# Optimization experiments

Measured on AMD Instinct MI355X. Metric: run time of the kernel, lower is better.

The kernel has to match this reference:

```python
import jax, jax.numpy as jnp
import numpy as np
from jax import lax


def _conv(x, w, b, pad, dil):
    # standard dense conv, NCHW / OIHW
    out = lax.conv_general_dilated(
        x, w, window_strides=(1, 1), padding=[(pad, pad), (pad, pad)],
        rhs_dilation=(dil, dil), dimension_numbers=('NCHW', 'OIHW', 'NCHW'))
    return out + b[None, :, None, None]


def _bilinear_sample(x, py, px):
    # x: [B,C,H,W]; py,px: [B,H,W] float coords. Zero padding outside bounds
    # (matches torchvision deform_conv2d bilinear sampling).
    B, C, H, W = x.shape
    y0 = jnp.floor(py)
    x0 = jnp.floor(px)
    wy = (py - y0)[:, None]  # [B,1,H,W]
    wx = (px - x0)[:, None]
    y0i = y0.astype(jnp.int32)
    x0i = x0.astype(jnp.int32)
    xf = x.reshape(B, C, H * W)

    def gather(yi, xi):
        valid = ((yi >= 0) & (yi < H) & (xi >= 0) & (xi < W))[:, None]
        yc = jnp.clip(yi, 0, H - 1)
        xc = jnp.clip(xi, 0, W - 1)
        idx = jnp.broadcast_to((yc * W + xc).reshape(B, 1, H * W), (B, C, H * W))
        v = jnp.take_along_axis(xf, idx, axis=2).reshape(B, C, H, W)
        return v * valid.astype(x.dtype)

    v00 = gather(y0i, x0i)
    v01 = gather(y0i, x0i + 1)
    v10 = gather(y0i + 1, x0i)
    v11 = gather(y0i + 1, x0i + 1)
    return (v00 * (1 - wy) * (1 - wx) + v01 * (1 - wy) * wx
            + v10 * wy * (1 - wx) + v11 * wy * wx)


def _deform_dw_conv(x, off_w, off_b, dw_w, k, pad, dil):
    # offset net: regular conv -> [B, 2*k*k, H, W] (dy,dx per kernel tap)
    # then depthwise deformable conv with weight dw_w: [C,1,k,k], no bias.
    B, C, H, W = x.shape
    off = _conv(x, off_w, off_b, pad, dil).reshape(B, k * k, 2, H, W)
    ys = jnp.arange(H, dtype=x.dtype)[None, :, None]  # [1,H,1]
    xs = jnp.arange(W, dtype=x.dtype)[None, None, :]  # [1,1,W]
    out = jnp.zeros_like(x)
    for t in range(k * k):  # small fixed tap count (25 or 49)
        ki, kj = t // k, t % k
        py = ys - pad + ki * dil + off[:, t, 0]  # [B,H,W]
        px = xs - pad + kj * dil + off[:, t, 1]
        samp = _bilinear_sample(x, py, px)       # [B,C,H,W]
        out = out + samp * dw_w[:, 0, ki, kj][None, :, None, None]
    return out


def setup_inputs() -> dict:
    key = jax.random.key(0)
    ks = jax.random.split(key, 10)
    B, C, H, W = 8, 64, 128, 128
    x = jax.random.normal(ks[0], (B, C, H, W), dtype=jnp.float32)
    # conv0: DeformConv 5x5, pad=2, dil=1, depthwise
    off0_w = jax.random.normal(ks[1], (2 * 25, C, 5, 5), dtype=jnp.float32) * 0.01
    off0_b = jnp.zeros((2 * 25,), dtype=jnp.float32)
    dw0_w = jax.random.normal(ks[2], (C, 1, 5, 5), dtype=jnp.float32) * (1.0 / 5.0)
    # conv_spatial: DeformConv 7x7, pad=9, dil=3, depthwise
    off1_w = jax.random.normal(ks[3], (2 * 49, C, 7, 7), dtype=jnp.float32) * 0.01
    off1_b = jnp.zeros((2 * 49,), dtype=jnp.float32)
    dw1_w = jax.random.normal(ks[4], (C, 1, 7, 7), dtype=jnp.float32) * (1.0 / 7.0)
    # conv1: 1x1 dense conv with bias
    conv1_w = jax.random.normal(ks[5], (C, C, 1, 1), dtype=jnp.float32) * (1.0 / np.sqrt(C))
    conv1_b = jnp.zeros((C,), dtype=jnp.float32)
    return {"x": x, "off0_w": off0_w, "off0_b": off0_b, "dw0_w": dw0_w,
            "off1_w": off1_w, "off1_b": off1_b, "dw1_w": dw1_w,
            "conv1_w": conv1_w, "conv1_b": conv1_b}


def reference(x, off0_w, off0_b, dw0_w, off1_w, off1_b, dw1_w, conv1_w, conv1_b):
    u = x
    attn = _deform_dw_conv(x, off0_w, off0_b, dw0_w, k=5, pad=2, dil=1)
    attn = _deform_dw_conv(attn, off1_w, off1_b, dw1_w, k=7, pad=9, dil=3)
    attn = jnp.einsum('bchw,oc->bohw', attn, conv1_w[:, :, 0, 0]) + conv1_b[None, :, None, None]
    return u * attn
```

## Files before the change

kernel.cpp:

```cpp
#include <hip/hip_runtime.h>

#define Bb 8
#define C  64
#define Hh 128
#define Ww 128
#define HW (Hh * Ww)

typedef __attribute__((ext_vector_type(8))) short b16x8;
typedef __attribute__((ext_vector_type(4))) float f32x4;
typedef _Float16 f16x8 __attribute__((ext_vector_type(8)));
typedef _Float16 h2 __attribute__((ext_vector_type(2)));
typedef __fp16 fp16x2cv __attribute__((ext_vector_type(2)));

__device__ __forceinline__ ushort f2h(float f) {
    union { _Float16 h; ushort u; } z; z.h = (_Float16)f; return z.u;
}
__device__ __forceinline__ h2 u2h(uint u) {
    union { uint u; h2 h; } x; x.u = u; return x.h;
}
__device__ __forceinline__ uint h2u(h2 h) {
    union { uint u; h2 h; } x; x.h = h; return x.u;
}
__device__ __forceinline__ uint pkrtz_u(float a, float b) {
    union { fp16x2cv h; uint u; } z;
    z.h = __builtin_amdgcn_cvt_pkrtz(a, b); return z.u;
}
__device__ __forceinline__ f16x8 s2h8(b16x8 s) {
    union { b16x8 s; f16x8 h; } x; x.s = s; return x.h;
}

__global__ void pack_nhwc(const float* __restrict__ in, ushort* __restrict__ out) {
    __shared__ ushort t[64][65];
    const int bx = blockIdx.x;
    const int b = bx >> 8, rem = bx & 255, h = rem >> 1, w0 = (rem & 1) << 6;
    const int x = threadIdx.x, wl = x & 63, cs = x >> 6;
    const float* ip = in + (((size_t)b * 64) << 14) + (h << 7) + w0 + wl;
    #pragma unroll
    for (int i = 0; i < 16; ++i) {
        const int c = i * 4 + cs;
        t[wl][c] = f2h(ip[(size_t)c << 14]);
    }
    __syncthreads();
    ushort* op = out + ((size_t)((b * Hh + h) * Ww + w0)) * 64 + wl;
    #pragma unroll
    for (int i = 0; i < 16; ++i) {
        const int w = i * 4 + cs;
        op[(size_t)w * 64] = t[w][wl];
    }
}

__global__ void pack_w(const float* __restrict__ src, ushort* __restrict__ dst,
                       int OC, int OCP, int KK, int n) {
    const int idx = blockIdx.x * 256 + threadIdx.x;
    if (idx >= n) return;
    const int kk = idx & 31;
    const int oc = (idx >> 5) % OCP;
    const int s = idx / (32 * OCP);
    const int c = (s & 1) * 32 + kk;
    const int t = s >> 1;
    const float v = (oc < OC) ? src[((size_t)oc * 64 + c) * KK + t] : 0.f;
    dst[idx] = f2h(v);
}

__global__ void pack_dwt(const float* __restrict__ src, ushort* __restrict__ dst, int KK) {
    const int i = blockIdx.x * 256 + threadIdx.x;
    if (i < KK * 64) {
        const int t = i >> 6, ch = i & 63;
        dst[i] = f2h(src[ch * KK + t]);
    }
}

template<int K, int PAD, int DIL, int OCP, int KR>
__global__ __launch_bounds__(256, 2) void conv_mfma(
    const ushort* __restrict__ xp,
    const ushort* __restrict__ wp,
    const float* __restrict__ bias,
    ushort* __restrict__ outp) {
    constexpr int WIDTH = 64 + (K - 1) * DIL;
    constexpr int S = 2 * K * K;
    constexpr int NT = OCP / 16;
    constexpr int TPW = (NT + 3) / 4;
    __shared__ __align__(16) ushort lds[KR * WIDTH * 64];

    const int bx = blockIdx.x;
    const int b = bx >> 8, rem = bx & 255, h = rem >> 1, w0 = (rem & 1) << 6;
    const int tid = threadIdx.x, lane = tid & 63, wid = tid >> 6;
    const int l15 = lane & 15, lg = lane >> 4;

    f32x4 acc[TPW][4] = {};

    const int nph = (K + KR - 1) / KR;
    for (int ph = 0; ph < nph; ++ph) {
        const int kr0 = ph * KR;
        const int krn = (K - kr0 < KR) ? (K - kr0) : KR;
        __syncthreads();
        const int chunks = krn * WIDTH * 8;
        for (int q = tid; q < chunks; q += 256) {
            const int ki = q / (WIDTH * 8);
            const int r2 = q - ki * (WIDTH * 8);
            const int widx = r2 >> 3, csl = r2 & 7;
            const int y = h - PAD + (kr0 + ki) * DIL;
            const int w = w0 - PAD + widx;
            uint4 v = make_uint4(0, 0, 0, 0);
            if ((unsigned)y < (unsigned)Hh && (unsigned)w < (unsigned)Ww)
                v = *(const uint4*)(xp + (((size_t)(b * Hh + y) * Ww + w) << 6) + (csl << 3));
            ((uint4*)lds)[(ki * WIDTH + widx) * 8 + (csl ^ (widx & 7))] = v;
        }
        __syncthreads();

        const int t0 = kr0 * K, t1 = (kr0 + krn) * K;
        for (int t = t0; t < t1; ++t) {
            const int ki = t / K - kr0;
            const int kj = t - (t / K) * K;
            const int s0 = 2 * t;
            b16x8 a[2][TPW];
            #pragma unroll
            for (int i = 0; i < TPW; ++i) {
                if (wid + 4 * i < NT) {
                    const int ot = wid + 4 * i;
                    const size_t abase = ((size_t)(ot * 16 + l15)) * 32 + lg * 8;
                    a[0][i] = *(const b16x8*)(wp + (size_t)s0 * (OCP * 32) + abase);
                    a[1][i] = *(const b16x8*)(wp + (size_t)(s0 + 1) * (OCP * 32) + abase);
                }
            }
            const int wbase = l15 + kj * DIL;
            int idx = (ki * WIDTH + wbase) * 8 + (lg ^ (wbase & 7));
            #pragma unroll
            for (int pt = 0; pt < 4; ++pt) {
                const b16x8 b0 = ((const b16x8*)lds)[idx];
                const b16x8 b1 = ((const b16x8*)lds)[idx ^ 4];
                #pragma unroll
                for (int i = 0; i < TPW; ++i) {
                    if (wid + 4 * i < NT) {
                        acc[i][pt] = __builtin_amdgcn_mfma_f32_16x16x32_f16(s2h8(a[0][i]), s2h8(b0), acc[i][pt], 0, 0, 0);
                        acc[i][pt] = __builtin_amdgcn_mfma_f32_16x16x32_f16(s2h8(a[1][i]), s2h8(b1), acc[i][pt], 0, 0, 0);
                    }
                }
                idx += 128;
            }
        }
    }

    __syncthreads();
    ushort* lo_ = lds;
    #pragma unroll
    for (int i = 0; i < TPW; ++i) {
        const int ot = wid + 4 * i;
        if (ot >= NT) continue;
        #pragma unroll
        for (int r = 0; r < 4; ++r) {
            const int oc = ot * 16 + lg * 4 + r;
            if (oc < S) {
                const float bv = bias[oc];
                #pragma unroll
                for (int pt = 0; pt < 4; ++pt)
                    lo_[(pt * 16 + l15) * S + oc] = f2h(acc[i][pt][r] + bv);
            }
        }
    }
    __syncthreads();
    const int nU = 64 * S / 2;
    uint* og = (uint*)outp + (size_t)((b * Hh + h) * Ww + w0) * (S / 2);
    for (int q = tid; q < nU; q += 256) og[q] = ((const uint*)lo_)[q];
}

template <int K, int PAD, int DIL>
__global__ __launch_bounds__(256) void deform4(
    const ushort* __restrict__ xp,
    const ushort* __restrict__ off,
    const ushort* __restrict__ dwt,
    ushort* __restrict__ outb) {
    constexpr int KK = K * K;
    __shared__ ushort dwl[KK * 64];
    __shared__ uint sIdx[32 * KK];
    __shared__ __align__(8) uint2 sW[32 * KK];
    const int tid = threadIdx.x;
    const int pix0 = blockIdx.x * 32;

    for (int i = tid; i < KK * 32; i += 256)
        ((uint*)dwl)[i] = ((const uint*)dwt)[i];

    const uint* og = (const uint*)off + (size_t)pix0 * KK;
    for (int q = tid; q < 32 * KK; q += 256) {
        const int pl2 = q / KK, t2 = q - pl2 * KK;
        const int pix = pix0 + pl2;
        const int h = (pix >> 7) & 127, w = pix & 127;
        const h2 oh = u2h(og[q]);
        const int ki = t2 / K, kj = t2 - ki * K;
        const float py = (float)(h - PAD + ki * DIL) + (float)oh.x;
        const float px = (float)(w - PAD + kj * DIL) + (float)oh.y;
        const float y0f = floorf(py), x0f = floorf(px);
        const float wy = py - y0f, wx = px - x0f;
        const int y0 = (int)y0f, x0 = (int)x0f;
        const int y1 = y0 + 1, x1 = x0 + 1;
        const float m00 = ((unsigned)y0 < 128u && (unsigned)x0 < 128u) ? 1.f : 0.f;
        const float m01 = ((unsigned)y0 < 128u && (unsigned)x1 < 128u) ? 1.f : 0.f;
        const float m10 = ((unsigned)y1 < 128u && (unsigned)x0 < 128u) ? 1.f : 0.f;
        const float m11 = ((unsigned)y1 < 128u && (unsigned)x1 < 128u) ? 1.f : 0.f;
        const int y0c = min(max(y0, 0), 127), y1c = min(max(y1, 0), 127);
        const int x0c = min(max(x0, 0), 127), x1c = min(max(x1, 0), 127);
        const float w00 = (1.f - wy) * (1.f - wx) * m00;
        const float w01 = (1.f - wy) * wx * m01;
        const float w10 = wy * (1.f - wx) * m10;
        const float w11 = wy * wx * m11;
        const int i00 = (y0c << 7) | x0c;
        const int i11 = (y1c << 7) | x1c;
        sIdx[q] = (uint)i00 | ((uint)i11 << 14);
        sW[q] = make_uint2(pkrtz_u(w00, w01), pkrtz_u(w10, w11));
    }
    __syncthreads();

    const int pl = tid >> 3, g = tid & 7;
    const int pix = pix0 + pl;
    const int b = pix0 >> 14;
    const int gb = g << 3;
    const ushort* xb = xp + ((size_t)b << 20);

    h2 acc_h[4] = {};

    for (int t = 0; t < KK; ++t) {
        const int sid = pl * KK + t;
        const uint id = sIdx[sid];
        const uint2 w4 = sW[sid];
        const h2 wA = u2h(w4.x), wB = u2h(w4.y);
        const h2 w00b = {wA.x, wA.x}, w01b = {wA.y, wA.y};
        const h2 w10b = {wB.x, wB.x}, w11b = {wB.y, wB.y};
        const int i00 = id & 16383;
        const int i11 = (id >> 14) & 16383;
        const int i01 = (i00 & ~127) | (i11 & 127);
        const int i10 = (i11 & ~127) | (i00 & 127);
        const uint4 qa = *(const uint4*)(xb + (i00 << 6) + gb);
        const uint4 qb = *(const uint4*)(xb + (i01 << 6) + gb);
        const uint4 qc = *(const uint4*)(xb + (i10 << 6) + gb);
        const uint4 qd = *(const uint4*)(xb + (i11 << 6) + gb);
        const uint4 dwv = *(const uint4*)(dwl + (t << 6) + gb);
        const uint* A = (const uint*)&qa;
        const uint* Bv = (const uint*)&qb;
        const uint* Cv = (const uint*)&qc;
        const uint* D = (const uint*)&qd;
        const uint* Dw = (const uint*)&dwv;
        #pragma unroll
        for (int j = 0; j < 4; ++j) {
            h2 v = u2h(A[j]) * w00b;
            v += u2h(Bv[j]) * w01b;
            v += u2h(Cv[j]) * w10b;
            v += u2h(D[j]) * w11b;
            acc_h[j] += v * u2h(Dw[j]);
        }
    }

    uint o4[4];
    #pragma unroll
    for (int j = 0; j < 4; ++j) o4[j] = h2u(acc_h[j]);
    *(uint4*)(outb + ((size_t)pix << 6) + gb) = *(uint4*)o4;
}

__global__ __launch_bounds__(256) void pw_mfma(
    const ushort* __restrict__ attn, const ushort* __restrict__ wp2,
    const float* __restrict__ b1, const float* __restrict__ x,
    float* __restrict__ out) {
    __shared__ __align__(16) ushort lds[64 * 64];
    const int tid = threadIdx.x, lane = tid & 63, wid = tid >> 6;
    const int l15 = lane & 15, lg = lane >> 4;
    const int pix0 = blockIdx.x << 6;

    const uint4* src = (const uint4*)(attn + ((size_t)pix0 << 6));
    for (int q = tid; q < 512; q += 256) {
        const int widx = q >> 3, csl = q & 7;
        ((uint4*)lds)[widx * 8 + (csl ^ (widx & 7))] = src[q];
    }
    __syncthreads();

    const b16x8 a0 = *(const b16x8*)(wp2 + ((size_t)(wid * 16 + l15)) * 32 + lg * 8);
    const b16x8 a1 = *(const b16x8*)(wp2 + ((size_t)(64 + wid * 16 + l15)) * 32 + lg * 8);
    f32x4 acc[4] = {};
    #pragma unroll
    for (int pt = 0; pt < 4; ++pt) {
        const int wb = pt * 16 + l15;
        const int idx = wb * 8 + (lg ^ (wb & 7));
        const b16x8 b0 = ((const b16x8*)lds)[idx];
        const b16x8 b1v = ((const b16x8*)lds)[idx ^ 4];
        acc[pt] = __builtin_amdgcn_mfma_f32_16x16x32_f16(s2h8(a0), s2h8(b0), acc[pt], 0, 0, 0);
        acc[pt] = __builtin_amdgcn_mfma_f32_16x16x32_f16(s2h8(a1), s2h8(b1v), acc[pt], 0, 0, 0);
    }

    const int b = pix0 >> 14, hw0 = pix0 & 16383;
    #pragma unroll
    for (int r = 0; r < 4; ++r) {
        const int oc = wid * 16 + lg * 4 + r;
        const float bv = b1[oc];
        const size_t base = (((size_t)b * 64 + oc) << 14) + hw0;
        #pragma unroll
        for (int pt = 0; pt < 4; ++pt) {
            const size_t oi = base + pt * 16 + l15;
            out[oi] = x[oi] * (acc[pt][r] + bv);
        }
    }
}

extern "C" void kernel_launch(void* const* d_in, const int* in_sizes, int n_in,
                              void* d_out, int out_size, void* d_ws, size_t ws_size,
                              hipStream_t stream) {
    const float* x       = (const float*)d_in[0];
    const float* off0_w  = (const float*)d_in[1];
    const float* off0_b  = (const float*)d_in[2];
    const float* dw0_w   = (const float*)d_in[3];
    const float* off1_w  = (const float*)d_in[4];
    const float* off1_b  = (const float*)d_in[5];
    const float* dw1_w   = (const float*)d_in[6];
    const float* conv1_w = (const float*)d_in[7];
    const float* conv1_b = (const float*)d_in[8];
    float* out = (float*)d_out;

    const size_t NPX = (size_t)Bb * HW;
    ushort* xp     = (ushort*)d_ws;
    ushort* attn0b = xp + NPX * 64;
    ushort* attn1b = attn0b + NPX * 64;
    ushort* offb   = attn1b + NPX * 64;
    ushort* wp0    = offb + NPX * 98;
    ushort* wp1    = wp0 + 50 * 64 * 32;
    ushort* wpP    = wp1 + 98 * 112 * 32;
    ushort* dwt0   = wpP + 2 * 64 * 32;
    ushort* dwt1   = dwt0 + 25 * 64;

    const dim3 blk(256);

    pack_nhwc<<<2048, blk, 0, stream>>>(x, xp);
    pack_w<<<(50 * 64 * 32 + 255) / 256, blk, 0, stream>>>(off0_w, wp0, 50, 64, 25, 50 * 64 * 32);
    pack_w<<<(98 * 112 * 32 + 255) / 256, blk, 0, stream>>>(off1_w, wp1, 98, 112, 49, 98 * 112 * 32);
    pack_w<<<16, blk, 0, stream>>>(conv1_w, wpP, 64, 64, 1, 2 * 64 * 32);
    pack_dwt<<<(25 * 64 + 255) / 256, blk, 0, stream>>>(dw0_w, dwt0, 25);
    pack_dwt<<<(49 * 64 + 255) / 256, blk, 0, stream>>>(dw1_w, dwt1, 49);

    conv_mfma<5, 2, 1, 64, 5><<<2048, blk, 0, stream>>>(xp, wp0, off0_b, offb);
    deform4<5, 2, 1><<<4096, blk, 0, stream>>>(xp, offb, dwt0, attn0b);

    conv_mfma<7, 9, 3, 112, 4><<<2048, blk, 0, stream>>>(attn0b, wp1, off1_b, offb);
    deform4<7, 9, 3><<<4096, blk, 0, stream>>>(attn0b, offb, dwt1, attn1b);

    pw_mfma<<<2048, blk, 0, stream>>>(attn1b, wpP, conv1_b, x, out);
}
```

Before: 352.8 us.

## Widen offset-conv tile to a full 128-pixel row with padded epilogue

Each conv_mfma block now covers a whole image row (128 pixels) instead of half a row. This doubles the accumulator tiles per wave, so each weight fragment loaded from global memory is reused across twice as many pixels. The input row-staging depth KR drops to 2, and launch bounds request 4 blocks per CU so the larger LDS footprint stays within occupancy limits. The epilogue pads the LDS row stride by one uint, likely to cut bank conflicts. The cost is higher register pressure from 8 accumulator sets and more staging phases with extra syncs.

New measurement: 312.1 us. 11.5% less time.

```diff
diff --git a/kernel.cpp b/kernel.cpp
--- a/kernel.cpp
+++ b/kernel.cpp
@@ -71,23 +71,27 @@
 }
 
 template<int K, int PAD, int DIL, int OCP, int KR>
-__global__ __launch_bounds__(256, 2) void conv_mfma(
+__global__ __launch_bounds__(256, 4) void conv_mfma(
     const ushort* __restrict__ xp,
     const ushort* __restrict__ wp,
     const float* __restrict__ bias,
     ushort* __restrict__ outp) {
-    constexpr int WIDTH = 64 + (K - 1) * DIL;
+    constexpr int WIDTH = 128 + (K - 1) * DIL;
     constexpr int S = 2 * K * K;
+    constexpr int SP = S + 2;
     constexpr int NT = OCP / 16;
     constexpr int TPW = (NT + 3) / 4;
-    __shared__ __align__(16) ushort lds[KR * WIDTH * 64];
+    constexpr int STG = KR * WIDTH * 64;
+    constexpr int EPI = 128 * SP;
+    constexpr int LN = STG > EPI ? STG : EPI;
+    __shared__ __align__(16) ushort lds[LN];
 
     const int bx = blockIdx.x;
-    const int b = bx >> 8, rem = bx & 255, h = rem >> 1, w0 = (rem & 1) << 6;
+    const int b = bx >> 7, h = bx & 127;
     const int tid = threadIdx.x, lane = tid & 63, wid = tid >> 6;
     const int l15 = lane & 15, lg = lane >> 4;
 
-    f32x4 acc[TPW][4] = {};
+    f32x4 acc[TPW][8] = {};
 
     const int nph = (K + KR - 1) / KR;
     for (int ph = 0; ph < nph; ++ph) {
@@ -100,16 +104,16 @@
             const int r2 = q - ki * (WIDTH * 8);
             const int widx = r2 >> 3, csl = r2 & 7;
             const int y = h - PAD + (kr0 + ki) * DIL;
-            const int w = w0 - PAD + widx;
+            const int w = -PAD + widx;
             uint4 v = make_uint4(0, 0, 0, 0);
-            if ((unsigned)y < (unsigned)Hh && (unsigned)w < (unsigned)Ww)
-                v = *(const uint4*)(xp + (((size_t)(b * Hh + y) * Ww + w) << 6) + (csl << 3));
+            if ((unsigned)y < 128u && (unsigned)w < 128u)
+                v = *(const uint4*)(xp + (((size_t)(b * 128 + y) * 128 + w) << 6) + (csl << 3));
             ((uint4*)lds)[(ki * WIDTH + widx) * 8 + (csl ^ (widx & 7))] = v;
         }
         __syncthreads();
 
-        const int t0 = kr0 * K, t1 = (kr0 + krn) * K;
-        for (int t = t0; t < t1; ++t) {
+        const int t1 = (kr0 + krn) * K;
+        for (int t = kr0 * K; t < t1; ++t) {
             const int ki = t / K - kr0;
             const int kj = t - (t / K) * K;
             const int s0 = 2 * t;
@@ -118,15 +122,15 @@
             for (int i = 0; i < TPW; ++i) {
                 if (wid + 4 * i < NT) {
                     const int ot = wid + 4 * i;
-                    const size_t abase = ((size_t)(ot * 16 + l15)) * 32 + lg * 8;
-                    a[0][i] = *(const b16x8*)(wp + (size_t)s0 * (OCP * 32) + abase);
-                    a[1][i] = *(const b16x8*)(wp + (size_t)(s0 + 1) * (OCP * 32) + abase);
+                    const size_t ab = ((size_t)(ot * 16 + l15)) * 32 + lg * 8;
+                    a[0][i] = *(const b16x8*)(wp + (size_t)s0 * (OCP * 32) + ab);
+                    a[1][i] = *(const b16x8*)(wp + (size_t)(s0 + 1) * (OCP * 32) + ab);
                 }
             }
-            const int wbase = l15 + kj * DIL;
-            int idx = (ki * WIDTH + wbase) * 8 + (lg ^ (wbase & 7));
+            const int wb0 = l15 + kj * DIL;
+            int idx = (ki * WIDTH + wb0) * 8 + (lg ^ (wb0 & 7));
             #pragma unroll
-            for (int pt = 0; pt < 4; ++pt) {
+            for (int pt = 0; pt < 8; ++pt) {
                 const b16x8 b0 = ((const b16x8*)lds)[idx];
                 const b16x8 b1 = ((const b16x8*)lds)[idx ^ 4];
                 #pragma unroll
@@ -142,7 +146,6 @@
     }
 
     __syncthreads();
-    ushort* lo_ = lds;
     #pragma unroll
     for (int i = 0; i < TPW; ++i) {
         const int ot = wid + 4 * i;
@@ -153,15 +156,19 @@
             if (oc < S) {
                 const float bv = bias[oc];
                 #pragma unroll
-                for (int pt = 0; pt < 4; ++pt)
-                    lo_[(pt * 16 + l15) * S + oc] = f2h(acc[i][pt][r] + bv);
+                for (int pt = 0; pt < 8; ++pt)
+                    lds[(pt * 16 + l15) * SP + oc] = f2h(acc[i][pt][r] + bv);
             }
         }
     }
     __syncthreads();
-    const int nU = 64 * S / 2;
-    uint* og = (uint*)outp + (size_t)((b * Hh + h) * Ww + w0) * (S / 2);
-    for (int q = tid; q < nU; q += 256) og[q] = ((const uint*)lo_)[q];
+    constexpr int SH = S / 2, SPH = SP / 2;
+    const uint* lu = (const uint*)lds;
+    uint* og = (uint*)outp + ((size_t)bx << 7) * SH;
+    for (int q = tid; q < 128 * SH; q += 256) {
+        const int pix = q / SH, s = q - pix * SH;
+        og[q] = lu[pix * SPH + s];
+    }
 }
 
 template <int K, int PAD, int DIL>
@@ -332,10 +339,10 @@
     pack_dwt<<<(25 * 64 + 255) / 256, blk, 0, stream>>>(dw0_w, dwt0, 25);
     pack_dwt<<<(49 * 64 + 255) / 256, blk, 0, stream>>>(dw1_w, dwt1, 49);
 
-    conv_mfma<5, 2, 1, 64, 5><<<2048, blk, 0, stream>>>(xp, wp0, off0_b, offb);
+    conv_mfma<5, 2, 1, 64, 2><<<1024, blk, 0, stream>>>(xp, wp0, off0_b, offb);
     deform4<5, 2, 1><<<4096, blk, 0, stream>>>(xp, offb, dwt0, attn0b);
 
-    conv_mfma<7, 9, 3, 112, 4><<<2048, blk, 0, stream>>>(attn0b, wp1, off1_b, offb);
+    conv_mfma<7, 9, 3, 112, 2><<<1024, blk, 0, stream>>>(attn0b, wp1, off1_b, offb);
     deform4<7, 9, 3><<<4096, blk, 0, stream>>>(attn0b, offb, dwt1, attn1b);
 
     pw_mfma<<<2048, blk, 0, stream>>>(attn1b, wpP, conv1_b, x, out);
```
